# Performance work log

Measured on AMD Instinct MI355X. Metric: run time of the kernel, lower is better.

The kernel has to match this reference:

```python
import jax, jax.numpy as jnp
import numpy as np

EPS = 1e-6  # AngularPhysicsConfig.eps


def setup_inputs() -> dict:
    key = jax.random.key(0)
    k1, k2 = jax.random.split(key)
    B, L, d, H = 2, 2048, 2048, 8
    x_spatial = jax.random.normal(k1, (B, L, d), dtype=jnp.float32)
    # attn is a softmax output: rows sum to 1 over the last axis
    attn = jax.nn.softmax(jax.random.normal(k2, (B, H, L, L), dtype=jnp.float32), axis=-1)
    W = jnp.ones((1,), dtype=jnp.float32)   # nn.Parameter(torch.ones(1))
    b = jnp.zeros((1,), dtype=jnp.float32)  # bias_init = 0.0
    return {"x_spatial": x_spatial, "attn": attn, "W": W, "b": b}


def reference(x_spatial, attn, W, b):
    # --- angular_kernel ---
    norm = jnp.clip(jnp.linalg.norm(x_spatial, axis=-1, keepdims=True), EPS, None)
    x_unit = x_spatial / norm                                   # [B, L, d]
    K = jnp.einsum('bld,bmd->blm', x_unit, x_unit)              # [B, L, L] cosine sim
    K_mean = K.mean(axis=(-1, -2), keepdims=True)
    K_cent = K - K_mean
    # torch .std() is unbiased (ddof=1), computed on detached K_cent
    K_std = jnp.std(jax.lax.stop_gradient(K_cent), axis=(-1, -2), keepdims=True, ddof=1)
    K_norm = K_cent / jnp.clip(K_std, EPS, None)                # [B, L, L]

    # --- compute_cos_align (detach_attn_for_alignment=True) ---
    A = jax.lax.stop_gradient(attn.mean(axis=1))                # [B, L, L]
    cos_align = jnp.sum(A * K_norm, axis=-1)                    # [B, L]

    # --- gate ---
    gate = jax.nn.sigmoid(W * cos_align + b)                    # [B, L]
    return gate, cos_align, K_norm
```

## Files before the change

### kernel.cpp

```cpp
#include <hip/hip_runtime.h>
#include <hip/hip_bf16.h>

#define L_DIM 2048
#define D_DIM 2048
#define B_DIM 2
#define H_DIM 8
#define NT 16
#define NPAIR 136
#define NRED 512
#define EPSV 1e-6f

using bf16x8 = __attribute__((ext_vector_type(8))) __bf16;
using f32x4  = __attribute__((ext_vector_type(4))) float;

__device__ inline void gload_lds16(const void* g, void* l) {
    __builtin_amdgcn_global_load_lds(
        (const __attribute__((address_space(1))) void*)g,
        (__attribute__((address_space(3))) void*)l, 16, 0, 0);
}

__device__ inline ushort f2bf(float f) {
    unsigned int u = __float_as_uint(f);
    unsigned int lsb = (u >> 16) & 1u;
    u += 0x7fffu + lsb;
    return (ushort)(u >> 16);
}
__device__ inline float bf2f(ushort u) {
    return __uint_as_float(((unsigned int)u) << 16);
}

__global__ __launch_bounds__(256) void k_normalize(const float* __restrict__ x,
                                                   ushort* __restrict__ xu,
                                                   double* __restrict__ sums) {
    const int row = blockIdx.x;
    const int t   = threadIdx.x;
    const float* xr = x + (size_t)row * D_DIM;
    float4 v0 = ((const float4*)xr)[t];
    float4 v1 = ((const float4*)xr)[t + 256];
    float ss = v0.x*v0.x + v0.y*v0.y + v0.z*v0.z + v0.w*v0.w
             + v1.x*v1.x + v1.y*v1.y + v1.z*v1.z + v1.w*v1.w;
    #pragma unroll
    for (int off = 32; off; off >>= 1) ss += __shfl_down(ss, off);
    __shared__ float red[4];
    __shared__ float s_inv;
    if ((t & 63) == 0) red[t >> 6] = ss;
    __syncthreads();
    if (t == 0) {
        float nrm = sqrtf(red[0] + red[1] + red[2] + red[3]);
        nrm = fmaxf(nrm, EPSV);
        s_inv = 1.0f / nrm;
        if (row == 0) { sums[0] = 0.0; sums[1] = 0.0; sums[2] = 0.0; sums[3] = 0.0; }
    }
    __syncthreads();
    const float inv = s_inv;
    ushort* xo = xu + (size_t)row * D_DIM;
    ushort4 o0, o1;
    o0.x = f2bf(v0.x * inv); o0.y = f2bf(v0.y * inv);
    o0.z = f2bf(v0.z * inv); o0.w = f2bf(v0.w * inv);
    o1.x = f2bf(v1.x * inv); o1.y = f2bf(v1.y * inv);
    o1.z = f2bf(v1.z * inv); o1.w = f2bf(v1.w * inv);
    ((ushort4*)xo)[t]       = o0;
    ((ushort4*)xo)[t + 256] = o1;
}

__global__ __launch_bounds__(256) void k_mixed(const ushort* __restrict__ Xu,
                                               const float* __restrict__ attn,
                                               float* __restrict__ Kout,
                                               double* __restrict__ sums,
                                               ushort* __restrict__ Amean) {
    __shared__ __align__(16) ushort lds_a[128 * 32];
    __shared__ __align__(16) ushort lds_b[128 * 32];
    const int t = threadIdx.x;
    const int batch = blockIdx.z;

    if (blockIdx.x >= NPAIR) {
        const int rid = blockIdx.x - NPAIR;
        const float* ab = attn + (size_t)batch * H_DIM * L_DIM * L_DIM;
        ushort* am = Amean + (size_t)batch * L_DIM * L_DIM;
        const int n4 = L_DIM * L_DIM / 4;
        for (int i = rid * 256 + t; i < n4; i += NRED * 256) {
            float4 s = {0.f, 0.f, 0.f, 0.f};
            #pragma unroll
            for (int h = 0; h < H_DIM; ++h) {
                const float4 v = ((const float4*)(ab + (size_t)h * L_DIM * L_DIM))[i];
                s.x += v.x; s.y += v.y; s.z += v.z; s.w += v.w;
            }
            ushort4 o;
            o.x = f2bf(s.x * 0.125f); o.y = f2bf(s.y * 0.125f);
            o.z = f2bf(s.z * 0.125f); o.w = f2bf(s.w * 0.125f);
            ((ushort4*)am)[i] = o;
        }
        return;
    }

    const int lane = t & 63;
    const int w    = t >> 6;
    const int wr   = w >> 1, wc = w & 1;
    int ti = 0, rem = blockIdx.x;
    while (rem >= NT - ti) { rem -= NT - ti; ++ti; }
    const int tj = ti + rem;
    const int bRow = ti * 128;
    const int bCol = tj * 128;
    const bool diag = (ti == tj);
    const ushort* Xb = Xu + (size_t)batch * L_DIM * D_DIM;

    const int srow = t >> 2;
    const int scol = ((t & 3) ^ (srow & 3)) * 8;
    const ushort* gA0 = Xb + (size_t)(bRow + srow)      * D_DIM + scol;
    const ushort* gA1 = Xb + (size_t)(bRow + 64 + srow) * D_DIM + scol;
    const ushort* gB0 = Xb + (size_t)(bCol + srow)      * D_DIM + scol;
    const ushort* gB1 = Xb + (size_t)(bCol + 64 + srow) * D_DIM + scol;
    ushort* lA0 = lds_a + t * 8;
    ushort* lA1 = lds_a + 64 * 32 + t * 8;
    ushort* lB0 = lds_b + t * 8;
    ushort* lB1 = lds_b + 64 * 32 + t * 8;

    f32x4 acc[4][4] = {};
    const int frow = lane & 15;
    const int fk   = lane >> 4;
    const int fx   = frow & 3;

    for (int kt = 0; kt < D_DIM / 32; ++kt) {
        __syncthreads();
        const size_t ko = (size_t)kt * 32;
        gload_lds16(gA0 + ko, lA0);
        gload_lds16(gA1 + ko, lA1);
        gload_lds16(gB0 + ko, lB0);
        gload_lds16(gB1 + ko, lB1);
        __syncthreads();
        bf16x8 a[4], b[4];
        #pragma unroll
        for (int m = 0; m < 4; ++m)
            a[m] = *(const bf16x8*)&lds_a[(wr * 64 + m * 16 + frow) * 32 + (fk ^ fx) * 8];
        #pragma unroll
        for (int n = 0; n < 4; ++n)
            b[n] = *(const bf16x8*)&lds_b[(wc * 64 + n * 16 + frow) * 32 + (fk ^ fx) * 8];
        #pragma unroll
        for (int m = 0; m < 4; ++m)
            #pragma unroll
            for (int n = 0; n < 4; ++n)
                acc[m][n] = __builtin_amdgcn_mfma_f32_16x16x32_bf16(a[m], b[n], acc[m][n], 0, 0, 0);
    }

    float* Kb = Kout + (size_t)batch * L_DIM * L_DIM;
    float ps = 0.f, pss = 0.f;
    #pragma unroll
    for (int m = 0; m < 4; ++m) {
        #pragma unroll
        for (int n = 0; n < 4; ++n) {
            #pragma unroll
            for (int j = 0; j < 4; ++j) {
                const int r = bRow + wr * 64 + m * 16 + fk * 4 + j;
                const int c = bCol + wc * 64 + n * 16 + frow;
                const float v = acc[m][n][j];
                Kb[(size_t)r * L_DIM + c] = v;
                ps += v; pss += v * v;
            }
            if (!diag) {
                const int rr  = bCol + wc * 64 + n * 16 + frow;
                const int cc0 = bRow + wr * 64 + m * 16 + fk * 4;
                *(float4*)&Kb[(size_t)rr * L_DIM + cc0] = *(float4*)&acc[m][n];
            }
        }
    }
    if (!diag) { ps *= 2.f; pss *= 2.f; }
    #pragma unroll
    for (int off = 32; off; off >>= 1) {
        ps  += __shfl_down(ps, off);
        pss += __shfl_down(pss, off);
    }
    __shared__ float redS[4], redSS[4];
    if (lane == 0) { redS[w] = ps; redSS[w] = pss; }
    __syncthreads();
    if (t == 0) {
        atomicAdd(&sums[batch * 2],     (double)(redS[0] + redS[1] + redS[2] + redS[3]));
        atomicAdd(&sums[batch * 2 + 1], (double)(redSS[0] + redSS[1] + redSS[2] + redSS[3]));
    }
}

__global__ __launch_bounds__(256) void k_epilogue(float* __restrict__ out,
                                                  const ushort* __restrict__ Amean,
                                                  const double* __restrict__ sums,
                                                  const float* __restrict__ Wp,
                                                  const float* __restrict__ bp) {
    const int row = blockIdx.x;
    const int b = row >> 11;
    const int t = threadIdx.x;

    const double N = (double)L_DIM * (double)L_DIM;
    const double mean_d = sums[b * 2] / N;
    double var = (sums[b * 2 + 1] - N * mean_d * mean_d) / (N - 1.0);
    var = var > 0.0 ? var : 0.0;
    float sd = (float)sqrt(var);
    sd = fmaxf(sd, EPSV);
    const float inv_std = 1.0f / sd;
    const float mean = (float)mean_d;

    float* Krow = out + 2 * B_DIM * L_DIM + (size_t)row * L_DIM;
    const ushort* arow = Amean + (size_t)row * L_DIM;

    float4 k0 = ((const float4*)Krow)[t * 2];
    float4 k1 = ((const float4*)Krow)[t * 2 + 1];
    const ushort4 a0 = ((const ushort4*)arow)[t * 2];
    const ushort4 a1 = ((const ushort4*)arow)[t * 2 + 1];
    float dot = bf2f(a0.x) * k0.x + bf2f(a0.y) * k0.y + bf2f(a0.z) * k0.z + bf2f(a0.w) * k0.w
              + bf2f(a1.x) * k1.x + bf2f(a1.y) * k1.y + bf2f(a1.z) * k1.z + bf2f(a1.w) * k1.w;
    float4 n0, n1;
    n0.x = (k0.x - mean) * inv_std; n0.y = (k0.y - mean) * inv_std;
    n0.z = (k0.z - mean) * inv_std; n0.w = (k0.w - mean) * inv_std;
    n1.x = (k1.x - mean) * inv_std; n1.y = (k1.y - mean) * inv_std;
    n1.z = (k1.z - mean) * inv_std; n1.w = (k1.w - mean) * inv_std;
    ((float4*)Krow)[t * 2]     = n0;
    ((float4*)Krow)[t * 2 + 1] = n1;

    #pragma unroll
    for (int off = 32; off; off >>= 1) dot += __shfl_down(dot, off);
    __shared__ float red[4];
    if ((t & 63) == 0) red[t >> 6] = dot;
    __syncthreads();
    if (t == 0) {
        const float dotv = red[0] + red[1] + red[2] + red[3];
        const float ca = (dotv - mean) * inv_std;
        out[B_DIM * L_DIM + row] = ca;
        const float z = Wp[0] * ca + bp[0];
        out[row] = 1.0f / (1.0f + expf(-z));
    }
}

extern "C" void kernel_launch(void* const* d_in, const int* in_sizes, int n_in,
                              void* d_out, int out_size, void* d_ws, size_t ws_size,
                              hipStream_t stream) {
    const float* x    = (const float*)d_in[0];
    const float* attn = (const float*)d_in[1];
    const float* W    = (const float*)d_in[2];
    const float* bb   = (const float*)d_in[3];
    float* out = (float*)d_out;

    const size_t XU_BYTES = (size_t)B_DIM * L_DIM * D_DIM * 2;
    ushort* xu    = (ushort*)d_ws;
    double* sums  = (double*)((char*)d_ws + XU_BYTES);
    ushort* Amean = (ushort*)((char*)d_ws + XU_BYTES + 256);
    float*  Kbuf  = out + 2 * B_DIM * L_DIM;

    hipLaunchKernelGGL(k_normalize, dim3(B_DIM * L_DIM), dim3(256), 0, stream,
                       x, xu, sums);
    hipLaunchKernelGGL(k_mixed, dim3(NPAIR + NRED, 1, B_DIM), dim3(256), 0, stream,
                       xu, attn, Kbuf, sums, Amean);
    hipLaunchKernelGGL(k_epilogue, dim3(B_DIM * L_DIM), dim3(256), 0, stream,
                       out, Amean, sums, W, bb);
}
```

Baseline: 122.7 us.

## Double-buffer LDS tiles in the Gram GEMM and change swizzle pattern

Splits the LDS A/B tiles into two buffers so the global-to-LDS load of the next K slice is issued before the MFMAs on the current slice run. This cuts the K loop from two barriers per step to one and hides load latency behind compute. The XOR swizzle now uses (row>>1)&3 to change the LDS bank mapping for the fragment reads. LDS use doubles, which may lower occupancy. Correctness relies on the global_load_lds completing before the barrier, with no explicit vmcnt wait.

Result: no change. 122.1 us (-0.5%).

```diff
diff --git a/kernel.cpp b/kernel.cpp
--- a/kernel.cpp
+++ b/kernel.cpp
@@ -8,6 +8,7 @@
 #define NT 16
 #define NPAIR 136
 #define NRED 512
+#define NKT (D_DIM / 32)
 #define EPSV 1e-6f
 
 using bf16x8 = __attribute__((ext_vector_type(8))) __bf16;
@@ -68,8 +69,8 @@
                                                float* __restrict__ Kout,
                                                double* __restrict__ sums,
                                                ushort* __restrict__ Amean) {
-    __shared__ __align__(16) ushort lds_a[128 * 32];
-    __shared__ __align__(16) ushort lds_b[128 * 32];
+    __shared__ __align__(16) ushort lds_a[2][128 * 32];
+    __shared__ __align__(16) ushort lds_b[2][128 * 32];
     const int t = threadIdx.x;
     const int batch = blockIdx.z;
 
@@ -105,41 +106,49 @@
     const ushort* Xb = Xu + (size_t)batch * L_DIM * D_DIM;
 
     const int srow = t >> 2;
-    const int scol = ((t & 3) ^ (srow & 3)) * 8;
+    const int scol = ((t & 3) ^ ((srow >> 1) & 3)) * 8;
     const ushort* gA0 = Xb + (size_t)(bRow + srow)      * D_DIM + scol;
     const ushort* gA1 = Xb + (size_t)(bRow + 64 + srow) * D_DIM + scol;
     const ushort* gB0 = Xb + (size_t)(bCol + srow)      * D_DIM + scol;
     const ushort* gB1 = Xb + (size_t)(bCol + 64 + srow) * D_DIM + scol;
-    ushort* lA0 = lds_a + t * 8;
-    ushort* lA1 = lds_a + 64 * 32 + t * 8;
-    ushort* lB0 = lds_b + t * 8;
-    ushort* lB1 = lds_b + 64 * 32 + t * 8;
+    const int ldst = t * 8;
 
     f32x4 acc[4][4] = {};
     const int frow = lane & 15;
     const int fk   = lane >> 4;
-    const int fx   = frow & 3;
-
-    for (int kt = 0; kt < D_DIM / 32; ++kt) {
-        __syncthreads();
+    const int fx   = (frow >> 1) & 3;
+
+    auto STAGE = [&](int buf, int kt) {
         const size_t ko = (size_t)kt * 32;
-        gload_lds16(gA0 + ko, lA0);
-        gload_lds16(gA1 + ko, lA1);
-        gload_lds16(gB0 + ko, lB0);
-        gload_lds16(gB1 + ko, lB1);
-        __syncthreads();
+        gload_lds16(gA0 + ko, &lds_a[buf][ldst]);
+        gload_lds16(gA1 + ko, &lds_a[buf][64 * 32 + ldst]);
+        gload_lds16(gB0 + ko, &lds_b[buf][ldst]);
+        gload_lds16(gB1 + ko, &lds_b[buf][64 * 32 + ldst]);
+    };
+    auto COMPUTE = [&](int buf) {
         bf16x8 a[4], b[4];
         #pragma unroll
         for (int m = 0; m < 4; ++m)
-            a[m] = *(const bf16x8*)&lds_a[(wr * 64 + m * 16 + frow) * 32 + (fk ^ fx) * 8];
+            a[m] = *(const bf16x8*)&lds_a[buf][(wr * 64 + m * 16 + frow) * 32 + (fk ^ fx) * 8];
         #pragma unroll
         for (int n = 0; n < 4; ++n)
-            b[n] = *(const bf16x8*)&lds_b[(wc * 64 + n * 16 + frow) * 32 + (fk ^ fx) * 8];
+            b[n] = *(const bf16x8*)&lds_b[buf][(wc * 64 + n * 16 + frow) * 32 + (fk ^ fx) * 8];
         #pragma unroll
         for (int m = 0; m < 4; ++m)
             #pragma unroll
             for (int n = 0; n < 4; ++n)
                 acc[m][n] = __builtin_amdgcn_mfma_f32_16x16x32_bf16(a[m], b[n], acc[m][n], 0, 0, 0);
+    };
+
+    STAGE(0, 0);
+    __syncthreads();
+    for (int kt = 0; kt < NKT; kt += 2) {
+        STAGE(1, kt + 1);
+        COMPUTE(0);
+        __syncthreads();
+        if (kt + 2 < NKT) STAGE(0, kt + 2);
+        COMPUTE(1);
+        __syncthreads();
     }
 
     float* Kb = Kout + (size_t)batch * L_DIM * L_DIM;
```
